# Optimization experiments

Measured on AMD Instinct MI355X. Metric: run time of the kernel, lower is better.

Reference implementation:

```python
import jax, jax.numpy as jnp
import numpy as np

N = 50000
E = 800000
IN_DIM = 6
HID = 32
HEADS = 2
NEG_SLOPE = 0.2


def setup_inputs() -> dict:
    key = jax.random.key(0)
    ks = jax.random.split(key, 12)
    x = jax.random.normal(ks[0], (N, IN_DIM), dtype=jnp.float32)
    edge_index = jax.random.randint(ks[1], (2, E), 0, N, dtype=jnp.int64)
    s = 0.1
    W1 = jax.random.normal(ks[2], (IN_DIM, HEADS * HID), jnp.float32) * s
    a_src1 = jax.random.normal(ks[3], (HEADS, HID), jnp.float32) * s
    a_dst1 = jax.random.normal(ks[4], (HEADS, HID), jnp.float32) * s
    b1 = jnp.zeros((HEADS * HID,), jnp.float32)
    W2 = jax.random.normal(ks[5], (HEADS * HID, HID), jnp.float32) * s
    a_src2 = jax.random.normal(ks[6], (1, HID), jnp.float32) * s
    a_dst2 = jax.random.normal(ks[7], (1, HID), jnp.float32) * s
    b2 = jnp.zeros((HID,), jnp.float32)
    Wout = jax.random.normal(ks[8], (HID, 1), jnp.float32) * s
    bout = jnp.zeros((1,), jnp.float32)
    return {"x": x, "edge_index": edge_index, "W1": W1, "a_src1": a_src1,
            "a_dst1": a_dst1, "b1": b1, "W2": W2, "a_src2": a_src2,
            "a_dst2": a_dst2, "b2": b2, "Wout": Wout, "bout": bout}


def gat_conv(x, src, dst, n, W, a_src, a_dst, b, heads, out_ch, concat):
    # x: [N, F_in]; src/dst: [E'] (self-loops already appended)
    h = (x @ W).reshape(n, heads, out_ch)              # [N, H, C]
    alpha_s = jnp.sum(h * a_src, axis=-1)              # [N, H]
    alpha_d = jnp.sum(h * a_dst, axis=-1)              # [N, H]
    e = jax.nn.leaky_relu(alpha_s[src] + alpha_d[dst], NEG_SLOPE)  # [E', H]
    # segment softmax over incoming edges of each destination node
    m = jax.ops.segment_max(e, dst, num_segments=n)    # [N, H]
    ex = jnp.exp(e - m[dst])
    denom = jax.ops.segment_sum(ex, dst, num_segments=n)
    alpha = ex / denom[dst]                            # [E', H]
    out = jax.ops.segment_sum(alpha[:, :, None] * h[src], dst, num_segments=n)  # [N, H, C]
    out = out.reshape(n, heads * out_ch) if concat else out.mean(axis=1)
    return out + b


def reference(x, edge_index, W1, a_src1, a_dst1, b1, W2, a_src2, a_dst2, b2, Wout, bout):
    n = x.shape[0]
    loops = jnp.arange(n, dtype=edge_index.dtype)
    src = jnp.concatenate([edge_index[0], loops])
    dst = jnp.concatenate([edge_index[1], loops])
    h = jax.nn.relu(gat_conv(x, src, dst, n, W1, a_src1, a_dst1, b1, HEADS, HID, True))
    h = jax.nn.relu(gat_conv(h, src, dst, n, W2, a_src2, a_dst2, b2, 1, HID, False))
    return jax.nn.sigmoid(h @ Wout + bout).squeeze(-1)  # [N]
```

## Files before the change

### kernel.cpp

```cpp
#include <hip/hip_runtime.h>

#define N_NODES 50000
#define N_EDGES 800000
#define ETOT    (N_EDGES + N_NODES)
#define NEG_SLOPE 0.2f
#define NBIN    ((N_NODES + 255) / 256)
#define CHUNK   4096
#define B_COARSE ((ETOT + CHUNK - 1) / CHUNK)

__device__ __forceinline__ float leaky(float v) {
    return v > 0.f ? v : NEG_SLOPE * v;
}

__device__ __forceinline__ void edge_src_dst(const int* ei, int e, int& src, int& dst) {
    if (e < N_EDGES) { src = ei[e]; dst = ei[N_EDGES + e]; }
    else             { src = dst = e - N_EDGES; }
}

__global__ void k_chist(const int* __restrict__ ei, int* __restrict__ bh) {
    __shared__ int h[NBIN];
    for (int i = threadIdx.x; i < NBIN; i += 256) h[i] = 0;
    __syncthreads();
    int base = blockIdx.x * CHUNK;
    int lim = min(base + CHUNK, ETOT);
    for (int e = base + threadIdx.x; e < lim; e += 256) {
        int s, d; edge_src_dst(ei, e, s, d);
        atomicAdd(&h[d >> 8], 1);
    }
    __syncthreads();
    for (int i = threadIdx.x; i < NBIN; i += 256)
        bh[i * B_COARSE + blockIdx.x] = h[i];
}

__global__ void k_cscan(int* __restrict__ bh, int* __restrict__ binoff) {
    __shared__ int s[256];
    int t = threadIdx.x;
    int run = 0;
    if (t < NBIN) {
        for (int b = 0; b < B_COARSE; ++b) {
            int v = bh[t * B_COARSE + b];
            bh[t * B_COARSE + b] = run;
            run += v;
        }
    }
    int v = (t < NBIN) ? run : 0;
    int x = v;
    s[t] = x;
    __syncthreads();
#pragma unroll
    for (int o = 1; o < 256; o <<= 1) {
        int tt = (t >= o) ? s[t - o] : 0;
        __syncthreads();
        x += tt;
        s[t] = x;
        __syncthreads();
    }
    if (t < NBIN) binoff[t] = x - v;
    if (t == 255) binoff[NBIN] = x;
}

__global__ void k_cscatter(const int* __restrict__ ei, const int* __restrict__ bh,
                           const int* __restrict__ binoff, unsigned* __restrict__ ebin) {
    __shared__ int cur[NBIN];
    for (int i = threadIdx.x; i < NBIN; i += 256)
        cur[i] = bh[i * B_COARSE + blockIdx.x] + binoff[i];
    __syncthreads();
    int base = blockIdx.x * CHUNK;
    int lim = min(base + CHUNK, ETOT);
    for (int e = base + threadIdx.x; e < lim; e += 256) {
        int s, d; edge_src_dst(ei, e, s, d);
        int pos = atomicAdd(&cur[d >> 8], 1);
        ebin[pos] = ((unsigned)s << 8) | (unsigned)(d & 255);
    }
}

__global__ void k_fine(const unsigned* __restrict__ ebin, const int* __restrict__ binoff,
                       int* __restrict__ rowstart, int* __restrict__ csr_src) {
    __shared__ int h[256];
    __shared__ int cur[256];
    int bin = blockIdx.x;
    int beg = binoff[bin], end = binoff[bin + 1];
    int t = threadIdx.x;
    h[t] = 0;
    __syncthreads();
    for (int i = beg + t; i < end; i += 256)
        atomicAdd(&h[ebin[i] & 255u], 1);
    __syncthreads();
    int v = h[t];
    int x = v;
    cur[t] = x;
    __syncthreads();
#pragma unroll
    for (int o = 1; o < 256; o <<= 1) {
        int tt = (t >= o) ? cur[t - o] : 0;
        __syncthreads();
        x += tt;
        cur[t] = x;
        __syncthreads();
    }
    int start = beg + x - v;
    int node = bin * 256 + t;
    if (node < N_NODES) rowstart[node] = start;
    if (bin == NBIN - 1 && t == 0) rowstart[N_NODES] = ETOT;
    cur[t] = start;
    __syncthreads();
    for (int i = beg + t; i < end; i += 256) {
        unsigned p = ebin[i];
        int pos = atomicAdd(&cur[p & 255u], 1);
        csr_src[pos] = (int)(p >> 8);
    }
}

__global__ void k_node1(const float* __restrict__ x, const float* __restrict__ W1,
                        const float* __restrict__ a_src1, const float* __restrict__ a_dst1,
                        float* __restrict__ as1, float* __restrict__ ad1) {
    int node = blockIdx.x * 4 + (threadIdx.x >> 6);
    if (node >= N_NODES) return;
    int j = threadIdx.x & 63;
    int head = j >> 5;

    float h = 0.f;
#pragma unroll
    for (int k = 0; k < 6; ++k)
        h += x[node * 6 + k] * W1[k * 64 + j];

    float s = h * a_src1[j];
    float d = h * a_dst1[j];
#pragma unroll
    for (int m = 1; m < 32; m <<= 1) {
        s += __shfl_xor(s, m);
        d += __shfl_xor(d, m);
    }
    if ((j & 31) == 0) {
        as1[node * 2 + head] = s;
        ad1[node * 2 + head] = d;
    }
}

__global__ void k_gat1(const int* __restrict__ csr_src, const int* __restrict__ rowstart,
                       const float* __restrict__ as1, const float* __restrict__ ad1,
                       const float* __restrict__ x, const float* __restrict__ W1,
                       const float* __restrict__ b1, float* __restrict__ o1) {
    int node = blockIdx.x * 16 + (threadIdx.x >> 4);
    if (node >= N_NODES) return;
    int l = threadIdx.x & 15;

    float p[4][6];
    float bv[4];
#pragma unroll
    for (int m = 0; m < 4; ++m) {
        int c = l + 16 * m;
#pragma unroll
        for (int k = 0; k < 6; ++k)
            p[m][k] = W1[k * 64 + c];
        bv[m] = b1[c];
    }

    int beg = rowstart[node], end = rowstart[node + 1];
    float2 adv = ((const float2*)ad1)[node];

    float a0 = 0, a1 = 0, a2 = 0, a3 = 0, a4 = 0, a5 = 0;
    float c0 = 0, c1 = 0, c2 = 0, c3 = 0, c4 = 0, c5 = 0;
    float dp0 = 0, dp1 = 0;
    for (int i = beg + l; i < end; i += 16) {
        int s = csr_src[i];
        float2 aa = ((const float2*)as1)[s];
        float w0 = __expf(leaky(aa.x + adv.x));
        float w1 = __expf(leaky(aa.y + adv.y));
        dp0 += w0;
        dp1 += w1;
        const float2* xs = (const float2*)(x + s * 6);
        float2 u = xs[0], v = xs[1], w = xs[2];
        a0 += w0 * u.x; a1 += w0 * u.y; a2 += w0 * v.x;
        a3 += w0 * v.y; a4 += w0 * w.x; a5 += w0 * w.y;
        c0 += w1 * u.x; c1 += w1 * u.y; c2 += w1 * v.x;
        c3 += w1 * v.y; c4 += w1 * w.x; c5 += w1 * w.y;
    }
#pragma unroll
    for (int o = 8; o; o >>= 1) {
        a0 += __shfl_xor(a0, o); a1 += __shfl_xor(a1, o); a2 += __shfl_xor(a2, o);
        a3 += __shfl_xor(a3, o); a4 += __shfl_xor(a4, o); a5 += __shfl_xor(a5, o);
        c0 += __shfl_xor(c0, o); c1 += __shfl_xor(c1, o); c2 += __shfl_xor(c2, o);
        c3 += __shfl_xor(c3, o); c4 += __shfl_xor(c4, o); c5 += __shfl_xor(c5, o);
        dp0 += __shfl_xor(dp0, o); dp1 += __shfl_xor(dp1, o);
    }
    float inv0 = 1.f / dp0;
    float inv1 = 1.f / dp1;
    float* ob = o1 + (size_t)node * 64;
#pragma unroll
    for (int m = 0; m < 4; ++m) {
        float dot;
        if (m < 2)
            dot = a0 * p[m][0] + a1 * p[m][1] + a2 * p[m][2]
                + a3 * p[m][3] + a4 * p[m][4] + a5 * p[m][5];
        else
            dot = c0 * p[m][0] + c1 * p[m][1] + c2 * p[m][2]
                + c3 * p[m][3] + c4 * p[m][4] + c5 * p[m][5];
        float v = dot * (m < 2 ? inv0 : inv1) + bv[m];
        ob[l + 16 * m] = v > 0.f ? v : 0.f;
    }
}

__global__ void k_node2(const float* __restrict__ o1, const float* __restrict__ W2,
                        const float* __restrict__ a_src2, const float* __restrict__ a_dst2,
                        float* __restrict__ h2, float* __restrict__ as2,
                        float* __restrict__ ad2) {
    __shared__ float W2s[64 * 32];
    for (int i = threadIdx.x; i < 64 * 32; i += 256)
        W2s[i] = W2[i];
    __syncthreads();

    int node = blockIdx.x * 8 + (threadIdx.x >> 5);
    if (node >= N_NODES) return;
    int j = threadIdx.x & 31;

    float acc = 0.f;
#pragma unroll
    for (int k = 0; k < 64; ++k)
        acc += o1[node * 64 + k] * W2s[k * 32 + j];
    h2[node * 32 + j] = acc;

    float s = acc * a_src2[j];
    float d = acc * a_dst2[j];
#pragma unroll
    for (int m = 1; m < 32; m <<= 1) {
        s += __shfl_xor(s, m, 32);
        d += __shfl_xor(d, m, 32);
    }
    if (j == 0) {
        as2[node] = s;
        ad2[node] = d;
    }
}

__global__ void k_gat2(const int* __restrict__ csr_src, const int* __restrict__ rowstart,
                       const float* __restrict__ as2, const float* __restrict__ ad2,
                       const float* __restrict__ h2, const float* __restrict__ b2,
                       const float* __restrict__ Wout, const float* __restrict__ bout,
                       float* __restrict__ out) {
    int node = blockIdx.x * 4 + (threadIdx.x >> 6);
    if (node >= N_NODES) return;
    int j = threadIdx.x & 63;
    int f = j & 31;
    int half = j >> 5;
    int beg = rowstart[node], end = rowstart[node + 1];
    float adv = ad2[node];

    float acc = 0.f, dp = 0.f;
    for (int base = beg; base < end; base += 64) {
        int idx = base + j;
        int cnt = min(64, end - base);
        float w = 0.f;
        int s = 0;
        if (idx < end) {
            s = csr_src[idx];
            w = __expf(leaky(as2[s] + adv));
            dp += w;
        }
        int k = 0;
        for (; k + 8 <= cnt; k += 8) {
#pragma unroll
            for (int u = 0; u < 4; ++u) {
                int   sk = __shfl(s, k + 2 * u + half);
                float wk = __shfl(w, k + 2 * u + half);
                acc += wk * h2[sk * 32 + f];
            }
        }
        for (; k + 2 <= cnt; k += 2) {
            int   sk = __shfl(s, k + half);
            float wk = __shfl(w, k + half);
            acc += wk * h2[sk * 32 + f];
        }
        if (k < cnt) {
            int   sk = __shfl(s, k);
            float wk = __shfl(w, k);
            if (half == 0) acc += wk * h2[sk * 32 + f];
        }
    }
#pragma unroll
    for (int o = 32; o; o >>= 1)
        dp += __shfl_xor(dp, o);
    acc += __shfl_xor(acc, 32);

    float v = acc / dp + b2[f];
    v = v > 0.f ? v : 0.f;
    float t = v * Wout[f];
#pragma unroll
    for (int o = 16; o; o >>= 1)
        t += __shfl_xor(t, o);
    if (j == 0)
        out[node] = 1.f / (1.f + __expf(-(t + bout[0])));
}

extern "C" void kernel_launch(void* const* d_in, const int* in_sizes, int n_in,
                              void* d_out, int out_size, void* d_ws, size_t ws_size,
                              hipStream_t stream) {
    const float* x    = (const float*)d_in[0];
    const int*   ei   = (const int*)  d_in[1];
    const float* W1   = (const float*)d_in[2];
    const float* asw1 = (const float*)d_in[3];
    const float* adw1 = (const float*)d_in[4];
    const float* b1   = (const float*)d_in[5];
    const float* W2   = (const float*)d_in[6];
    const float* asw2 = (const float*)d_in[7];
    const float* adw2 = (const float*)d_in[8];
    const float* b2   = (const float*)d_in[9];
    const float* Wout = (const float*)d_in[10];
    const float* bout = (const float*)d_in[11];
    float* out = (float*)d_out;

    char* p = (char*)d_ws;
    auto carve = [&](size_t bytes) {
        void* r = (void*)p;
        p += (bytes + 255) & ~size_t(255);
        return r;
    };
    float*    o1       = (float*)   carve((size_t)N_NODES * 64 * 4);
    float*    h2       = (float*)   carve((size_t)N_NODES * 32 * 4);
    float*    as1      = (float*)   carve((size_t)N_NODES * 2 * 4);
    float*    ad1      = (float*)   carve((size_t)N_NODES * 2 * 4);
    float*    as2      = (float*)   carve((size_t)N_NODES * 4);
    float*    ad2      = (float*)   carve((size_t)N_NODES * 4);
    int*      bh       = (int*)     carve((size_t)NBIN * B_COARSE * 4);
    int*      binoff   = (int*)     carve((size_t)(NBIN + 1) * 4);
    unsigned* ebin     = (unsigned*)carve((size_t)ETOT * 4);
    int*      rowstart = (int*)     carve((size_t)(N_NODES + 1) * 4);
    int*      csr_src  = (int*)     carve((size_t)ETOT * 4);

    const int TB = 256;

    k_chist   <<<B_COARSE, TB, 0, stream>>>(ei, bh);
    k_cscan   <<<1, TB, 0, stream>>>(bh, binoff);
    k_cscatter<<<B_COARSE, TB, 0, stream>>>(ei, bh, binoff, ebin);
    k_fine    <<<NBIN, TB, 0, stream>>>(ebin, binoff, rowstart, csr_src);

    k_node1<<<(N_NODES + 3) / 4, TB, 0, stream>>>(x, W1, asw1, adw1, as1, ad1);
    k_gat1 <<<(N_NODES + 15) / 16, TB, 0, stream>>>(csr_src, rowstart, as1, ad1, x, W1, b1, o1);

    k_node2<<<(N_NODES + 7) / 8, TB, 0, stream>>>(o1, W2, asw2, adw2, h2, as2, ad2);
    k_gat2 <<<(N_NODES + 3) / 4, TB, 0, stream>>>(csr_src, rowstart, as2, ad2, h2, b2, Wout, bout, out);
}
```

Baseline: 117.6 us.

## Store layer-2 features in fp16, fuse node1 into histogram kernel, transpose bin counts

Layer-2 node features h2 are stored as fp16, and the gather kernel is reworked so each lane reads a half2 and handles four edges per step. This halves gather traffic in the dominant aggregation kernel. The node1 attention-coefficient computation is merged into the coarse histogram launch as extra blocks, saving one kernel launch. The per-block bin histogram is stored transposed for coalesced writes. fp16 storage adds rounding error to h2, and the final 2-element remainder handling is now implicit through padding lanes with weight 0.

```diff
diff --git a/kernel.cpp b/kernel.cpp
--- a/kernel.cpp
+++ b/kernel.cpp
@@ -1,4 +1,5 @@
 #include <hip/hip_runtime.h>
+#include <hip/hip_fp16.h>
 
 #define N_NODES 50000
 #define N_EDGES 800000
@@ -7,6 +8,7 @@
 #define NBIN    ((N_NODES + 255) / 256)
 #define CHUNK   4096
 #define B_COARSE ((ETOT + CHUNK - 1) / CHUNK)
+#define G_NODE1 ((N_NODES + 3) / 4)
 
 __device__ __forceinline__ float leaky(float v) {
     return v > 0.f ? v : NEG_SLOPE * v;
@@ -17,19 +19,45 @@
     else             { src = dst = e - N_EDGES; }
 }
 
-__global__ void k_chist(const int* __restrict__ ei, int* __restrict__ bh) {
+__global__ void k_pre(const float* __restrict__ x, const float* __restrict__ W1,
+                      const float* __restrict__ a_src1, const float* __restrict__ a_dst1,
+                      float* __restrict__ as1, float* __restrict__ ad1,
+                      const int* __restrict__ ei, int* __restrict__ bh) {
     __shared__ int h[NBIN];
-    for (int i = threadIdx.x; i < NBIN; i += 256) h[i] = 0;
-    __syncthreads();
-    int base = blockIdx.x * CHUNK;
-    int lim = min(base + CHUNK, ETOT);
-    for (int e = base + threadIdx.x; e < lim; e += 256) {
-        int s, d; edge_src_dst(ei, e, s, d);
-        atomicAdd(&h[d >> 8], 1);
-    }
-    __syncthreads();
-    for (int i = threadIdx.x; i < NBIN; i += 256)
-        bh[i * B_COARSE + blockIdx.x] = h[i];
+    if (blockIdx.x < G_NODE1) {
+        int node = blockIdx.x * 4 + (threadIdx.x >> 6);
+        if (node >= N_NODES) return;
+        int j = threadIdx.x & 63;
+        int head = j >> 5;
+        float hv = 0.f;
+#pragma unroll
+        for (int k = 0; k < 6; ++k)
+            hv += x[node * 6 + k] * W1[k * 64 + j];
+        float s = hv * a_src1[j];
+        float d = hv * a_dst1[j];
+#pragma unroll
+        for (int m = 1; m < 32; m <<= 1) {
+            s += __shfl_xor(s, m);
+            d += __shfl_xor(d, m);
+        }
+        if ((j & 31) == 0) {
+            as1[node * 2 + head] = s;
+            ad1[node * 2 + head] = d;
+        }
+    } else {
+        int b = blockIdx.x - G_NODE1;
+        for (int i = threadIdx.x; i < NBIN; i += 256) h[i] = 0;
+        __syncthreads();
+        int base = b * CHUNK;
+        int lim = min(base + CHUNK, ETOT);
+        for (int e = base + threadIdx.x; e < lim; e += 256) {
+            int s, d; edge_src_dst(ei, e, s, d);
+            atomicAdd(&h[d >> 8], 1);
+        }
+        __syncthreads();
+        for (int i = threadIdx.x; i < NBIN; i += 256)
+            bh[b * NBIN + i] = h[i];
+    }
 }
 
 __global__ void k_cscan(int* __restrict__ bh, int* __restrict__ binoff) {
@@ -38,8 +66,8 @@
     int run = 0;
     if (t < NBIN) {
         for (int b = 0; b < B_COARSE; ++b) {
-            int v = bh[t * B_COARSE + b];
-            bh[t * B_COARSE + b] = run;
+            int v = bh[b * NBIN + t];
+            bh[b * NBIN + t] = run;
             run += v;
         }
     }
@@ -63,7 +91,7 @@
                            const int* __restrict__ binoff, unsigned* __restrict__ ebin) {
     __shared__ int cur[NBIN];
     for (int i = threadIdx.x; i < NBIN; i += 256)
-        cur[i] = bh[i * B_COARSE + blockIdx.x] + binoff[i];
+        cur[i] = bh[blockIdx.x * NBIN + i] + binoff[i];
     __syncthreads();
     int base = blockIdx.x * CHUNK;
     int lim = min(base + CHUNK, ETOT);
@@ -108,32 +136,6 @@
         unsigned p = ebin[i];
         int pos = atomicAdd(&cur[p & 255u], 1);
         csr_src[pos] = (int)(p >> 8);
-    }
-}
-
-__global__ void k_node1(const float* __restrict__ x, const float* __restrict__ W1,
-                        const float* __restrict__ a_src1, const float* __restrict__ a_dst1,
-                        float* __restrict__ as1, float* __restrict__ ad1) {
-    int node = blockIdx.x * 4 + (threadIdx.x >> 6);
-    if (node >= N_NODES) return;
-    int j = threadIdx.x & 63;
-    int head = j >> 5;
-
-    float h = 0.f;
-#pragma unroll
-    for (int k = 0; k < 6; ++k)
-        h += x[node * 6 + k] * W1[k * 64 + j];
-
-    float s = h * a_src1[j];
-    float d = h * a_dst1[j];
-#pragma unroll
-    for (int m = 1; m < 32; m <<= 1) {
-        s += __shfl_xor(s, m);
-        d += __shfl_xor(d, m);
-    }
-    if ((j & 31) == 0) {
-        as1[node * 2 + head] = s;
-        ad1[node * 2 + head] = d;
     }
 }
 
@@ -203,7 +205,7 @@
 
 __global__ void k_node2(const float* __restrict__ o1, const float* __restrict__ W2,
                         const float* __restrict__ a_src2, const float* __restrict__ a_dst2,
-                        float* __restrict__ h2, float* __restrict__ as2,
+                        __half* __restrict__ h2h, float* __restrict__ as2,
                         float* __restrict__ ad2) {
     __shared__ float W2s[64 * 32];
     for (int i = threadIdx.x; i < 64 * 32; i += 256)
@@ -218,7 +220,7 @@
 #pragma unroll
     for (int k = 0; k < 64; ++k)
         acc += o1[node * 64 + k] * W2s[k * 32 + j];
-    h2[node * 32 + j] = acc;
+    h2h[node * 32 + j] = __float2half(acc);
 
     float s = acc * a_src2[j];
     float d = acc * a_dst2[j];
@@ -235,21 +237,20 @@
 
 __global__ void k_gat2(const int* __restrict__ csr_src, const int* __restrict__ rowstart,
                        const float* __restrict__ as2, const float* __restrict__ ad2,
-                       const float* __restrict__ h2, const float* __restrict__ b2,
+                       const __half2* __restrict__ h2h, const float* __restrict__ b2,
                        const float* __restrict__ Wout, const float* __restrict__ bout,
                        float* __restrict__ out) {
     int node = blockIdx.x * 4 + (threadIdx.x >> 6);
     if (node >= N_NODES) return;
     int j = threadIdx.x & 63;
-    int f = j & 31;
-    int half = j >> 5;
+    int f = j & 15;
+    int slot = j >> 4;
     int beg = rowstart[node], end = rowstart[node + 1];
     float adv = ad2[node];
 
-    float acc = 0.f, dp = 0.f;
+    float accx = 0.f, accy = 0.f, dp = 0.f;
     for (int base = beg; base < end; base += 64) {
         int idx = base + j;
-        int cnt = min(64, end - base);
         float w = 0.f;
         int s = 0;
         if (idx < end) {
@@ -257,36 +258,29 @@
             w = __expf(leaky(as2[s] + adv));
             dp += w;
         }
-        int k = 0;
-        for (; k + 8 <= cnt; k += 8) {
-#pragma unroll
-            for (int u = 0; u < 4; ++u) {
-                int   sk = __shfl(s, k + 2 * u + half);
-                float wk = __shfl(w, k + 2 * u + half);
-                acc += wk * h2[sk * 32 + f];
-            }
-        }
-        for (; k + 2 <= cnt; k += 2) {
-            int   sk = __shfl(s, k + half);
-            float wk = __shfl(w, k + half);
-            acc += wk * h2[sk * 32 + f];
-        }
-        if (k < cnt) {
-            int   sk = __shfl(s, k);
-            float wk = __shfl(w, k);
-            if (half == 0) acc += wk * h2[sk * 32 + f];
+        int cnt = min(64, end - base);
+        for (int k = 0; k < cnt; k += 4) {
+            int   sk = __shfl(s, k + slot);
+            float wk = __shfl(w, k + slot);
+            float2 hv = __half22float2(h2h[sk * 16 + f]);
+            accx += wk * hv.x;
+            accy += wk * hv.y;
         }
     }
 #pragma unroll
     for (int o = 32; o; o >>= 1)
         dp += __shfl_xor(dp, o);
-    acc += __shfl_xor(acc, 32);
-
-    float v = acc / dp + b2[f];
-    v = v > 0.f ? v : 0.f;
-    float t = v * Wout[f];
-#pragma unroll
-    for (int o = 16; o; o >>= 1)
+    accx += __shfl_xor(accx, 16); accy += __shfl_xor(accy, 16);
+    accx += __shfl_xor(accx, 32); accy += __shfl_xor(accy, 32);
+
+    float inv = 1.f / dp;
+    float vx = accx * inv + b2[2 * f];
+    float vy = accy * inv + b2[2 * f + 1];
+    vx = vx > 0.f ? vx : 0.f;
+    vy = vy > 0.f ? vy : 0.f;
+    float t = vx * Wout[2 * f] + vy * Wout[2 * f + 1];
+#pragma unroll
+    for (int o = 8; o; o >>= 1)
         t += __shfl_xor(t, o);
     if (j == 0)
         out[node] = 1.f / (1.f + __expf(-(t + bout[0])));
@@ -316,12 +310,12 @@
         return r;
     };
     float*    o1       = (float*)   carve((size_t)N_NODES * 64 * 4);
-    float*    h2       = (float*)   carve((size_t)N_NODES * 32 * 4);
+    __half*   h2h      = (__half*)  carve((size_t)N_NODES * 32 * 2);
     float*    as1      = (float*)   carve((size_t)N_NODES * 2 * 4);
     float*    ad1      = (float*)   carve((size_t)N_NODES * 2 * 4);
     float*    as2      = (float*)   carve((size_t)N_NODES * 4);
     float*    ad2      = (float*)   carve((size_t)N_NODES * 4);
-    int*      bh       = (int*)     carve((size_t)NBIN * B_COARSE * 4);
+    int*      bh       = (int*)     carve((size_t)B_COARSE * NBIN * 4);
     int*      binoff   = (int*)     carve((size_t)(NBIN + 1) * 4);
     unsigned* ebin     = (unsigned*)carve((size_t)ETOT * 4);
     int*      rowstart = (int*)     carve((size_t)(N_NODES + 1) * 4);
@@ -329,14 +323,14 @@
 
     const int TB = 256;
 
-    k_chist   <<<B_COARSE, TB, 0, stream>>>(ei, bh);
+    k_pre     <<<G_NODE1 + B_COARSE, TB, 0, stream>>>(x, W1, asw1, adw1, as1, ad1, ei, bh);
     k_cscan   <<<1, TB, 0, stream>>>(bh, binoff);
     k_cscatter<<<B_COARSE, TB, 0, stream>>>(ei, bh, binoff, ebin);
     k_fine    <<<NBIN, TB, 0, stream>>>(ebin, binoff, rowstart, csr_src);
 
-    k_node1<<<(N_NODES + 3) / 4, TB, 0, stream>>>(x, W1, asw1, adw1, as1, ad1);
     k_gat1 <<<(N_NODES + 15) / 16, TB, 0, stream>>>(csr_src, rowstart, as1, ad1, x, W1, b1, o1);
 
-    k_node2<<<(N_NODES + 7) / 8, TB, 0, stream>>>(o1, W2, asw2, adw2, h2, as2, ad2);
-    k_gat2 <<<(N_NODES + 3) / 4, TB, 0, stream>>>(csr_src, rowstart, as2, ad2, h2, b2, Wout, bout, out);
-}
+    k_node2<<<(N_NODES + 7) / 8, TB, 0, stream>>>(o1, W2, asw2, adw2, h2h, as2, ad2);
+    k_gat2 <<<(N_NODES + 3) / 4, TB, 0, stream>>>(csr_src, rowstart, as2, ad2,
+                                                  (const __half2*)h2h, b2, Wout, bout, out);
+}
```

Result: faster. 106.8 us (-9.2%).
